# Kernel tuning notes

Hardware: AMD Instinct MI355X
Metric: run time of the kernel (lower is better)

The kernel has to match this reference:

```python
import jax, jax.numpy as jnp
import numpy as np

P = 32          # patch_size (window side); N = P*P tokens
C = 192         # dim
HEADS = 12
HD = C // HEADS # 16
HIDDEN = C * 4  # mlp_ratio=4
SCALE = HD ** -0.5


def _conv(x, w, b, pad):
    y = jax.lax.conv_general_dilated(
        x, w, window_strides=(1, 1), padding=[(pad, pad), (pad, pad)],
        dimension_numbers=("NCHW", "OIHW", "NCHW"))
    return y + b[None, :, None, None]


def setup_inputs() -> dict:
    key = jax.random.key(0)
    ks = jax.random.split(key, 8)
    B = 16
    x = jax.random.normal(ks[0], (B, P * P, C), dtype=jnp.float32)
    w1 = jax.random.normal(ks[1], (HIDDEN, C, 3, 3), dtype=jnp.float32) * 0.05
    b1 = jnp.zeros((HIDDEN,), dtype=jnp.float32)
    w2 = jax.random.normal(ks[2], (HIDDEN, HIDDEN, 1, 1), dtype=jnp.float32) * 0.05
    b2 = jnp.zeros((HIDDEN,), dtype=jnp.float32)
    w3 = jax.random.normal(ks[3], (3 * C, HIDDEN, 1, 1), dtype=jnp.float32) * 0.05
    b3 = jnp.zeros((3 * C,), dtype=jnp.float32)
    w_out = jax.random.normal(ks[4], (C, C), dtype=jnp.float32) * (C ** -0.5)
    return {"x": x, "w1": w1, "b1": b1, "w2": w2, "b2": b2,
            "w3": w3, "b3": b3, "w_out": w_out}


def reference(x, w1, b1, w2, b2, w3, b3, w_out):
    B, N, _ = x.shape
    # [B,N,C] -> [B,C,P,P] (NCHW image per window)
    xi = jnp.transpose(x.reshape(B, P, P, C), (0, 3, 1, 2))
    # F.unfold(x, P, stride=P): single block -> [B, 1, C*P*P] (C-major flatten)
    y = xi.reshape(B, 1, C * P * P)
    # LAConv.attention1: conv3x3 -> relu -> conv1x1 -> relu -> conv1x1 -> sigmoid
    a = jax.nn.relu(_conv(xi, w1, b1, 1))
    a = jax.nn.relu(_conv(a, w2, b2, 0))
    a = jax.nn.sigmoid(_conv(a, w3, b3, 0))          # [B, 3C, P, P]
    # reshape(B,3C,1,P,1,P).permute(0,2,4,3,5,1).view(B,1,P*P*3C)
    a = jnp.transpose(a.reshape(B, 3 * C, 1, P, 1, P), (0, 2, 4, 3, 5, 1))
    a = a.reshape(B, 1, P * P * 3 * C)
    qc, kc, vc = jnp.split(a, 3, axis=-1)            # each [B, 1, P*P*C]

    def to_heads(c):
        # (chunk * unfold) -> [B,P,P,C] -> [B,C,P,P] -> heads view [B,H,N,hd]
        t = jnp.transpose((c * y).reshape(B, P, P, C), (0, 3, 1, 2))
        return jnp.transpose(t.reshape(B, N, HEADS, HD), (0, 2, 1, 3))

    q = to_heads(qc) * SCALE
    k = to_heads(kc)
    v = to_heads(vc)
    attn = jax.nn.softmax(jnp.einsum("bhnd,bhmd->bhnm", q, k), axis=-1)
    o = jnp.einsum("bhnm,bhmd->bhnd", attn, v)
    o = jnp.transpose(o, (0, 2, 1, 3)).reshape(B, N, C)
    return o @ w_out.T


if __name__ == "__main__":
    out = reference(**setup_inputs())
    print(out.shape)
```

## Files before the change

kernel.cpp:

```cpp
#include <hip/hip_runtime.h>
#include <hip/hip_bf16.h>
#include <math.h>

#define B_   16
#define P_   32
#define N_   1024
#define C_   192
#define H_   12
#define HD_  16
#define HID_ 768
#define C3_  576
#define SCALE_ 0.25f

using u16 = unsigned short;
typedef __bf16 bf16x8 __attribute__((ext_vector_type(8)));
typedef float f32x4 __attribute__((ext_vector_type(4)));
typedef u16 u16x8 __attribute__((ext_vector_type(8)));
typedef u16 u16x4 __attribute__((ext_vector_type(4)));

#define MFMA16(a, b, c) __builtin_amdgcn_mfma_f32_16x16x32_bf16((a), (b), (c), 0, 0, 0)

__device__ __forceinline__ int swz(int r) { return (r + (r >> 2)) & 3; }

__device__ __forceinline__ void splitf(float v, u16& h, u16& l) {
  union { __hip_bfloat16 b; u16 u; } c1, c2;
  c1.b = __float2bfloat16(v);
  float hv = __bfloat162float(c1.b);
  c2.b = __float2bfloat16(v - hv);
  h = c1.u; l = c2.u;
}

__device__ __forceinline__ u16 bfbits(float v) {
  union { __hip_bfloat16 b; u16 u; } c; c.b = __float2bfloat16(v); return c.u;
}

__device__ __forceinline__ bf16x8 ldfrag(const u16* base, int row, int g) {
  return __builtin_bit_cast(bf16x8,
      *(const u16x8*)(base + row * 32 + ((g ^ swz(row)) << 3)));
}

__global__ __launch_bounds__(256) void pack_x_kernel(const float* __restrict__ x,
                                                     u16* __restrict__ xph,
                                                     u16* __restrict__ xpl) {
  int tid = blockIdx.x * 256 + threadIdx.x;
  int b = tid / 27744;
  int r = tid - b * 27744;
  int pp = r / 24;
  int cg = (r - pp * 24) * 8;
  int pr = pp / 34, pc = pp - pr * 34;
  float v[8] = {0.f, 0.f, 0.f, 0.f, 0.f, 0.f, 0.f, 0.f};
  if (pr >= 1 && pr <= 32 && pc >= 1 && pc <= 32) {
    const float* src = x + ((size_t)b * N_ + (pr - 1) * 32 + (pc - 1)) * C_ + cg;
    float4 v0 = *(const float4*)src;
    float4 v1 = *(const float4*)(src + 4);
    v[0] = v0.x; v[1] = v0.y; v[2] = v0.z; v[3] = v0.w;
    v[4] = v1.x; v[5] = v1.y; v[6] = v1.z; v[7] = v1.w;
  }
  u16x8 vh, vl;
#pragma unroll
  for (int i = 0; i < 8; ++i) { u16 h, l; splitf(v[i], h, l); vh[i] = h; vl[i] = l; }
  size_t o = ((size_t)b * 1156 + pp) * C_ + cg;
  *(u16x8*)&xph[o] = vh;
  *(u16x8*)&xpl[o] = vl;
}

__global__ __launch_bounds__(256) void pack_w1_kernel(const float* __restrict__ w1,
                                                      u16* __restrict__ w1h,
                                                      u16* __restrict__ w1l) {
  int tid = blockIdx.x * 256 + threadIdx.x;
  int oc = tid / C_, ic = tid - oc * C_;
  const float* src = w1 + ((size_t)oc * C_ + ic) * 9;
#pragma unroll
  for (int t9 = 0; t9 < 9; ++t9) {
    u16 h, l; splitf(src[t9], h, l);
    size_t o = (size_t)t9 * (HID_ * C_) + oc * C_ + ic;
    w1h[o] = h; w1l[o] = l;
  }
}

__global__ __launch_bounds__(256) void pack_gen_kernel(const float* __restrict__ src,
                                                       u16* __restrict__ dh,
                                                       u16* __restrict__ dl, int n8) {
  int tid = blockIdx.x * 256 + threadIdx.x;
  if (tid >= n8) return;
  const float* s = src + (size_t)tid * 8;
  float4 v0 = *(const float4*)s;
  float4 v1 = *(const float4*)(s + 4);
  float v[8] = {v0.x, v0.y, v0.z, v0.w, v1.x, v1.y, v1.z, v1.w};
  u16x8 vh, vl;
#pragma unroll
  for (int i = 0; i < 8; ++i) { u16 h, l; splitf(v[i], h, l); vh[i] = h; vl[i] = l; }
  *(u16x8*)&dh[(size_t)tid * 8] = vh;
  *(u16x8*)&dl[(size_t)tid * 8] = vl;
}

__global__ __launch_bounds__(256) void conv_mfma_kernel(
    const u16* __restrict__ xph, const u16* __restrict__ xpl,
    const u16* __restrict__ w1h, const u16* __restrict__ w1l,
    const float* __restrict__ b1, u16* __restrict__ a1h, u16* __restrict__ a1l) {
  __shared__ u16 sA[2][128 * 32];
  __shared__ u16 sB[2][128 * 32];
  int t = threadIdx.x;
  int n0 = blockIdx.x * 128, oc0 = blockIdx.y * 128, b = blockIdx.z;
  int wid = t >> 6, lane = t & 63;
  int wm = wid >> 1, wn = wid & 1;
  int g = lane >> 4, lr = lane & 15;
  f32x4 acc[4][4] = {};

  for (int tap = 0; tap < 9; ++tap) {
    int dy = tap / 3, dx = tap - dy * 3;
    const u16* wth = w1h + (size_t)tap * (HID_ * C_);
    const u16* wtl = w1l + (size_t)tap * (HID_ * C_);
    for (int ks = 0; ks < 6; ++ks) {
      int kk = ks * 32;
      __syncthreads();
#pragma unroll
      for (int i = 0; i < 2; ++i) {
        int c = t + i * 256;
        int r = c >> 2, p = c & 3;
        size_t gidx = (size_t)(oc0 + r) * C_ + kk + p * 8;
        int lidx = r * 32 + ((p ^ swz(r)) << 3);
        *(u16x8*)&sA[0][lidx] = *(const u16x8*)&wth[gidx];
        *(u16x8*)&sA[1][lidx] = *(const u16x8*)&wtl[gidx];
      }
#pragma unroll
      for (int i = 0; i < 2; ++i) {
        int c = t + i * 256;
        int r = c >> 2, p = c & 3;
        int pix = n0 + r;
        int py = pix >> 5, px = pix & 31;
        int pad = (py + dy) * 34 + (px + dx);
        size_t gidx = ((size_t)b * 1156 + pad) * C_ + kk + p * 8;
        int lidx = r * 32 + ((p ^ swz(r)) << 3);
        *(u16x8*)&sB[0][lidx] = *(const u16x8*)&xph[gidx];
        *(u16x8*)&sB[1][lidx] = *(const u16x8*)&xpl[gidx];
      }
      __syncthreads();
      bf16x8 ah[4], al[4], bh[4], bl[4];
#pragma unroll
      for (int mf = 0; mf < 4; ++mf) {
        int row = wm * 64 + mf * 16 + lr;
        ah[mf] = ldfrag(&sA[0][0], row, g);
        al[mf] = ldfrag(&sA[1][0], row, g);
      }
#pragma unroll
      for (int nf = 0; nf < 4; ++nf) {
        int row = wn * 64 + nf * 16 + lr;
        bh[nf] = ldfrag(&sB[0][0], row, g);
        bl[nf] = ldfrag(&sB[1][0], row, g);
      }
#pragma unroll
      for (int mf = 0; mf < 4; ++mf)
#pragma unroll
        for (int nf = 0; nf < 4; ++nf) {
          acc[mf][nf] = MFMA16(ah[mf], bh[nf], acc[mf][nf]);
          acc[mf][nf] = MFMA16(al[mf], bh[nf], acc[mf][nf]);
          acc[mf][nf] = MFMA16(ah[mf], bl[nf], acc[mf][nf]);
        }
    }
  }
#pragma unroll
  for (int mf = 0; mf < 4; ++mf)
#pragma unroll
    for (int nf = 0; nf < 4; ++nf) {
      int pix = n0 + wn * 64 + nf * 16 + lr;
      int oc = oc0 + wm * 64 + mf * 16 + g * 4;
      size_t oidx = ((size_t)b * N_ + pix) * HID_ + oc;
      u16x4 vh, vl;
#pragma unroll
      for (int r = 0; r < 4; ++r) {
        float v = acc[mf][nf][r] + b1[oc + r];
        v = v > 0.f ? v : 0.f;
        u16 h, l; splitf(v, h, l);
        vh[r] = h; vl[r] = l;
      }
      *(u16x4*)&a1h[oidx] = vh;
      *(u16x4*)&a1l[oidx] = vl;
    }
}

template <int ACT, int MT>
__global__ __launch_bounds__(256) void gemm_mfma_kernel(
    const u16* __restrict__ Wh, const u16* __restrict__ Wl,
    const float* __restrict__ bias,
    const u16* __restrict__ inh, const u16* __restrict__ inl,
    void* __restrict__ out0, void* __restrict__ out1, int OC, int IC) {
  constexpr int MF = MT / 32;
  __shared__ u16 sA[2][MT * 32];
  __shared__ u16 sB[2][128 * 32];
  int t = threadIdx.x;
  int n0 = blockIdx.x * 128, oc0 = blockIdx.y * MT, b = blockIdx.z;
  int wid = t >> 6, lane = t & 63;
  int wm = wid >> 1, wn = wid & 1;
  int g = lane >> 4, lr = lane & 15;
  const u16* inbh = inh + (size_t)b * N_ * IC;
  const u16* inbl = inl + (size_t)b * N_ * IC;
  f32x4 acc[MF][4] = {};

  for (int ks = 0; ks < IC / 32; ++ks) {
    int kk = ks * 32;
    __syncthreads();
    for (int c = t; c < MT * 4; c += 256) {
      int r = c >> 2, p = c & 3;
      size_t gidx = (size_t)(oc0 + r) * IC + kk + p * 8;
      int lidx = r * 32 + ((p ^ swz(r)) << 3);
      *(u16x8*)&sA[0][lidx] = *(const u16x8*)&Wh[gidx];
      *(u16x8*)&sA[1][lidx] = *(const u16x8*)&Wl[gidx];
    }
#pragma unroll
    for (int i = 0; i < 2; ++i) {
      int c = t + i * 256;
      int r = c >> 2, p = c & 3;
      size_t gidx = (size_t)(n0 + r) * IC + kk + p * 8;
      int lidx = r * 32 + ((p ^ swz(r)) << 3);
      *(u16x8*)&sB[0][lidx] = *(const u16x8*)&inbh[gidx];
      *(u16x8*)&sB[1][lidx] = *(const u16x8*)&inbl[gidx];
    }
    __syncthreads();
    bf16x8 ah[MF], al[MF], bh[4], bl[4];
#pragma unroll
    for (int mf = 0; mf < MF; ++mf) {
      int row = wm * (MT / 2) + mf * 16 + lr;
      ah[mf] = ldfrag(&sA[0][0], row, g);
      al[mf] = ldfrag(&sA[1][0], row, g);
    }
#pragma unroll
    for (int nf = 0; nf < 4; ++nf) {
      int row = wn * 64 + nf * 16 + lr;
      bh[nf] = ldfrag(&sB[0][0], row, g);
      bl[nf] = ldfrag(&sB[1][0], row, g);
    }
#pragma unroll
    for (int mf = 0; mf < MF; ++mf)
#pragma unroll
      for (int nf = 0; nf < 4; ++nf) {
        acc[mf][nf] = MFMA16(ah[mf], bh[nf], acc[mf][nf]);
        acc[mf][nf] = MFMA16(al[mf], bh[nf], acc[mf][nf]);
        acc[mf][nf] = MFMA16(ah[mf], bl[nf], acc[mf][nf]);
      }
  }
#pragma unroll
  for (int mf = 0; mf < MF; ++mf)
#pragma unroll
    for (int nf = 0; nf < 4; ++nf) {
      int pix = n0 + wn * 64 + nf * 16 + lr;
      int oc = oc0 + wm * (MT / 2) + mf * 16 + g * 4;
      size_t oidx = ((size_t)b * N_ + pix) * OC + oc;
      if constexpr (ACT == 0) {
        u16x4 vh, vl;
#pragma unroll
        for (int r = 0; r < 4; ++r) {
          float v = acc[mf][nf][r] + bias[oc + r];
          v = v > 0.f ? v : 0.f;
          u16 h, l; splitf(v, h, l);
          vh[r] = h; vl[r] = l;
        }
        *(u16x4*)&((u16*)out0)[oidx] = vh;
        *(u16x4*)&((u16*)out1)[oidx] = vl;
      } else if constexpr (ACT == 1) {
        float4 res;
        float r0 = acc[mf][nf][0] + bias[oc + 0];
        float r1 = acc[mf][nf][1] + bias[oc + 1];
        float r2 = acc[mf][nf][2] + bias[oc + 2];
        float r3 = acc[mf][nf][3] + bias[oc + 3];
        res.x = 1.f / (1.f + __expf(-r0)); res.y = 1.f / (1.f + __expf(-r1));
        res.z = 1.f / (1.f + __expf(-r2)); res.w = 1.f / (1.f + __expf(-r3));
        *(float4*)&((float*)out0)[oidx] = res;
      } else {
        float4 res;
        res.x = acc[mf][nf][0]; res.y = acc[mf][nf][1];
        res.z = acc[mf][nf][2]; res.w = acc[mf][nf][3];
        *(float4*)&((float*)out0)[oidx] = res;
      }
    }
}

__global__ __launch_bounds__(256) void qkv_gather_kernel(const float* __restrict__ a3,
                                                         const float* __restrict__ x,
                                                         u16* __restrict__ qh,
                                                         u16* __restrict__ ql,
                                                         u16* __restrict__ kh,
                                                         u16* __restrict__ kl,
                                                         u16* __restrict__ vb) {
  int idx = blockIdx.x * 256 + threadIdx.x;
  int b = idx / 196608;
  int gg = idx - b * 196608;
  int m = gg & 1023, cc = gg >> 10;
  int j = m * 192 + cc;
  float y = x[((size_t)b * N_ + (j & 1023)) * C_ + (j >> 10)];
  int n2 = gg / 192;
  int hd = gg - n2 * 192;
  size_t out_idx = (((size_t)b * H_ + (hd >> 4)) * N_ + n2) * HD_ + (hd & 15);
  const float* a3b = a3 + (size_t)b * (C3_ * N_);
  int jk = j + 196608, jv = j + 393216;
  int nq = j / 576,  chq = j - nq * 576;
  int nk = jk / 576, chk = jk - nk * 576;
  int nv = jv / 576, chv = jv - nv * 576;
  float aq = a3b[(size_t)nq * C3_ + chq];
  float ak = a3b[(size_t)nk * C3_ + chk];
  float av = a3b[(size_t)nv * C3_ + chv];
  u16 hh, ll;
  splitf(aq * y * SCALE_, hh, ll); qh[out_idx] = hh; ql[out_idx] = ll;
  splitf(ak * y, hh, ll);          kh[out_idx] = hh; kl[out_idx] = ll;
  vb[out_idx] = bfbits(av * y);
}

__global__ __launch_bounds__(256) void attn_mfma_kernel(
    const u16* __restrict__ QH, const u16* __restrict__ QL,
    const u16* __restrict__ KH, const u16* __restrict__ KL,
    const u16* __restrict__ VB, u16* __restrict__ oh, u16* __restrict__ ol) {
  __shared__ u16 sKH[128 * 32];
  __shared__ u16 sKL[128 * 32];
  __shared__ u16 sVT[16 * 128];
  __shared__ u16 sP[4][16 * 128];
  int t = threadIdx.x;
  int qt = blockIdx.x, h = blockIdx.y, b = blockIdx.z;
  int wid = t >> 6, lane = t & 63;
  int lr = lane & 15, g = lane >> 4;
  size_t base = ((size_t)(b * H_ + h)) * (N_ * HD_);
  int qrow = qt * 64 + wid * 16 + lr;

  {
    int plane = t >> 7, r = t & 127;
    u16* dst = (plane ? sKL : sKH) + r * 32;
    u16x8 z = {};
    *(u16x8*)(dst + ((2 ^ swz(r)) << 3)) = z;
    *(u16x8*)(dst + ((3 ^ swz(r)) << 3)) = z;
  }

  bf16x8 qfh = {}, qfl = {};
  if (g < 2) {
    size_t qi = base + (size_t)qrow * HD_ + g * 8;
    qfh = __builtin_bit_cast(bf16x8, *(const u16x8*)&QH[qi]);
    qfl = __builtin_bit_cast(bf16x8, *(const u16x8*)&QL[qi]);
  }

  f32x4 acc = {};
  float mrun = -1e30f, lrun = 0.f;
  u16* pw = &sP[wid][0];

  for (int ch = 0; ch < 8; ++ch) {
    int key0 = ch * 128;
    __syncthreads();
    {
      int plane = t >> 7, id = t & 127;
      const u16* kbase = (plane ? KL : KH) + base;
      u16* dstb = plane ? sKL : sKH;
#pragma unroll
      for (int i = 0; i < 2; ++i) {
        int e = i * 128 + id;
        int r = e >> 1, gg2 = e & 1;
        *(u16x8*)&dstb[r * 32 + ((gg2 ^ swz(r)) << 3)] =
            *(const u16x8*)&kbase[(size_t)(key0 + r) * HD_ + gg2 * 8];
      }
    }
#pragma unroll
    for (int i = 0; i < 2; ++i) {
      int e = i * 256 + t;
      int key = e >> 2, d0 = (e & 3) * 4;
      u16x4 vv = *(const u16x4*)&VB[base + (size_t)(key0 + key) * HD_ + d0];
#pragma unroll
      for (int jj = 0; jj < 4; ++jj) {
        int d = d0 + jj;
        sVT[d * 128 + (((key >> 3) ^ (d & 7)) << 3) + (key & 7)] = vv[jj];
      }
    }
    __syncthreads();

    f32x4 st[8];
#pragma unroll
    for (int t8 = 0; t8 < 8; ++t8) {
      bf16x8 kfh = ldfrag(sKH, t8 * 16 + lr, g);
      bf16x8 kfl = ldfrag(sKL, t8 * 16 + lr, g);
      f32x4 s = {};
      s = MFMA16(kfh, qfl, s);
      s = MFMA16(kfl, qfh, s);
      s = MFMA16(kfh, qfh, s);
      st[t8] = s;
    }

    float cmax = -1e30f;
#pragma unroll
    for (int t8 = 0; t8 < 8; ++t8)
#pragma unroll
      for (int r = 0; r < 4; ++r) cmax = fmaxf(cmax, st[t8][r]);
    cmax = fmaxf(cmax, __shfl_xor(cmax, 16));
    cmax = fmaxf(cmax, __shfl_xor(cmax, 32));
    float mnew = fmaxf(mrun, cmax);
    float corr = __expf(mrun - mnew);
    float p[32];
    float psum = 0.f;
#pragma unroll
    for (int t8 = 0; t8 < 8; ++t8)
#pragma unroll
      for (int r = 0; r < 4; ++r) {
        float pv = __expf(st[t8][r] - mnew);
        p[t8 * 4 + r] = pv; psum += pv;
      }
    psum += __shfl_xor(psum, 16);
    psum += __shfl_xor(psum, 32);
    lrun = lrun * corr + psum;
    mrun = mnew;
#pragma unroll
    for (int r = 0; r < 4; ++r) acc[r] *= corr;

#pragma unroll
    for (int t8 = 0; t8 < 8; ++t8) {
      unsigned w0 = (unsigned)bfbits(p[t8 * 4 + 0]) | ((unsigned)bfbits(p[t8 * 4 + 1]) << 16);
      unsigned w1 = (unsigned)bfbits(p[t8 * 4 + 2]) | ((unsigned)bfbits(p[t8 * 4 + 3]) << 16);
      int c = 2 * t8 + (g >> 1);
      int off = lr * 128 + ((c ^ (lr & 7)) << 3) + (g & 1) * 4;
      uint2 val; val.x = w0; val.y = w1;
      *(uint2*)&pw[off] = val;
    }
#pragma unroll
    for (int kk = 0; kk < 4; ++kk) {
      int off = lr * 128 + (((kk * 4 + g) ^ (lr & 7)) << 3);
      bf16x8 pb = __builtin_bit_cast(bf16x8, *(const u16x8*)&pw[off]);
      bf16x8 va = __builtin_bit_cast(bf16x8, *(const u16x8*)&sVT[off]);
      acc = MFMA16(va, pb, acc);
    }
  }

  float inv = 1.0f / lrun;
  size_t o = ((size_t)b * N_ + qrow) * C_ + h * HD_ + 4 * g;
  u16x4 vh, vl;
#pragma unroll
  for (int r = 0; r < 4; ++r) {
    u16 hh, ll; splitf(acc[r] * inv, hh, ll);
    vh[r] = hh; vl[r] = ll;
  }
  *(u16x4*)&oh[o] = vh;
  *(u16x4*)&ol[o] = vl;
}

extern "C" void kernel_launch(void* const* d_in, const int* in_sizes, int n_in,
                              void* d_out, int out_size, void* d_ws, size_t ws_size,
                              hipStream_t stream) {
  const float* x     = (const float*)d_in[0];
  const float* w1    = (const float*)d_in[1];
  const float* b1    = (const float*)d_in[2];
  const float* w2    = (const float*)d_in[3];
  const float* b2    = (const float*)d_in[4];
  const float* w3    = (const float*)d_in[5];
  const float* b3    = (const float*)d_in[6];
  const float* w_out = (const float*)d_in[7];
  float* out = (float*)d_out;

  char* ws = (char*)d_ws;
  u16* XPH = (u16*)(ws + 0);
  u16* XPL = (u16*)(ws + 7102464);
  u16* W1H = (u16*)(ws + 14204928);
  u16* W1L = (u16*)(ws + 16859136);
  u16* W2H = (u16*)(ws + 19513344);
  u16* W2L = (u16*)(ws + 20692992);
  u16* W3H = (u16*)(ws + 21872640);
  u16* W3L = (u16*)(ws + 22757376);
  u16* WOH = (u16*)(ws + 23642112);
  u16* WOL = (u16*)(ws + 23715840);
  u16*   A1H = (u16*)(ws + 23789568);
  u16*   A1L = (u16*)(ws + 48955392);
  float* A3  = (float*)(ws + 23789568);
  u16*   OH  = (u16*)(ws + 23789568);
  u16*   OL  = (u16*)(ws + 36372480);
  u16*   A2H = (u16*)(ws + 74121216);
  u16*   A2L = (u16*)(ws + 99287040);
  u16*   QHb = (u16*)(ws + 74121216);
  u16*   QLb = (u16*)(ws + 80412672);
  u16*   KHb = (u16*)(ws + 86704128);
  u16*   KLb = (u16*)(ws + 92995584);
  u16*   VBb = (u16*)(ws + 99287040);

  pack_x_kernel<<<dim3(1734), 256, 0, stream>>>(x, XPH, XPL);
  pack_w1_kernel<<<dim3(576), 256, 0, stream>>>(w1, W1H, W1L);
  pack_gen_kernel<<<dim3(288), 256, 0, stream>>>(w2, W2H, W2L, 73728);
  pack_gen_kernel<<<dim3(216), 256, 0, stream>>>(w3, W3H, W3L, 55296);
  pack_gen_kernel<<<dim3(18), 256, 0, stream>>>(w_out, WOH, WOL, 4608);

  conv_mfma_kernel<<<dim3(8, 6, 16), 256, 0, stream>>>(XPH, XPL, W1H, W1L, b1, A1H, A1L);
  gemm_mfma_kernel<0, 128><<<dim3(8, 6, 16), 256, 0, stream>>>(
      W2H, W2L, b2, A1H, A1L, A2H, A2L, HID_, HID_);
  gemm_mfma_kernel<1, 64><<<dim3(8, 9, 16), 256, 0, stream>>>(
      W3H, W3L, b3, A2H, A2L, A3, nullptr, C3_, HID_);
  qkv_gather_kernel<<<dim3(12288), 256, 0, stream>>>(A3, x, QHb, QLb, KHb, KLb, VBb);
  attn_mfma_kernel<<<dim3(16, 12, 16), 256, 0, stream>>>(QHb, QLb, KHb, KLb, VBb, OH, OL);
  gemm_mfma_kernel<2, 64><<<dim3(8, 3, 16), 256, 0, stream>>>(
      WOH, WOL, nullptr, OH, OL, out, nullptr, C_, C_);
}
```

Before: 498.1 us.

## Stage conv halo tile once per K-slice and read weights directly from global

The 3x3 conv kernel now loads a 6-row padded halo of the input (204 pixels) into shared memory once per 32-channel K-slice and reuses it across all 9 taps, instead of reloading a shifted input tile for every tap. Weight fragments in both the conv and the 1x1 GEMM kernels are now read straight from global memory into registers, which removes the shared-memory staging of the A operand. The conv kernel also gets a launch-bounds occupancy hint of 3 blocks per CU. The aim is fewer barriers and less global-to-LDS traffic, at the cost of uncoalesced, cache-dependent global weight loads inside the MFMA loop.

```diff
diff --git a/kernel.cpp b/kernel.cpp
--- a/kernel.cpp
+++ b/kernel.cpp
@@ -37,6 +37,10 @@
 __device__ __forceinline__ bf16x8 ldfrag(const u16* base, int row, int g) {
   return __builtin_bit_cast(bf16x8,
       *(const u16x8*)(base + row * 32 + ((g ^ swz(row)) << 3)));
+}
+
+__device__ __forceinline__ bf16x8 ldg8(const u16* p) {
+  return __builtin_bit_cast(bf16x8, *(const u16x8*)p);
 }
 
 __global__ __launch_bounds__(256) void pack_x_kernel(const float* __restrict__ x,
@@ -94,60 +98,49 @@
   *(u16x8*)&dl[(size_t)tid * 8] = vl;
 }
 
-__global__ __launch_bounds__(256) void conv_mfma_kernel(
+__global__ __launch_bounds__(256, 3) void conv_mfma_kernel(
     const u16* __restrict__ xph, const u16* __restrict__ xpl,
     const u16* __restrict__ w1h, const u16* __restrict__ w1l,
     const float* __restrict__ b1, u16* __restrict__ a1h, u16* __restrict__ a1l) {
-  __shared__ u16 sA[2][128 * 32];
-  __shared__ u16 sB[2][128 * 32];
+  __shared__ u16 sH[2][204 * 32];
   int t = threadIdx.x;
   int n0 = blockIdx.x * 128, oc0 = blockIdx.y * 128, b = blockIdx.z;
+  int row0 = blockIdx.x * 4;
   int wid = t >> 6, lane = t & 63;
   int wm = wid >> 1, wn = wid & 1;
   int g = lane >> 4, lr = lane & 15;
   f32x4 acc[4][4] = {};
 
-  for (int tap = 0; tap < 9; ++tap) {
-    int dy = tap / 3, dx = tap - dy * 3;
-    const u16* wth = w1h + (size_t)tap * (HID_ * C_);
-    const u16* wtl = w1l + (size_t)tap * (HID_ * C_);
-    for (int ks = 0; ks < 6; ++ks) {
-      int kk = ks * 32;
-      __syncthreads();
-#pragma unroll
-      for (int i = 0; i < 2; ++i) {
-        int c = t + i * 256;
-        int r = c >> 2, p = c & 3;
-        size_t gidx = (size_t)(oc0 + r) * C_ + kk + p * 8;
-        int lidx = r * 32 + ((p ^ swz(r)) << 3);
-        *(u16x8*)&sA[0][lidx] = *(const u16x8*)&wth[gidx];
-        *(u16x8*)&sA[1][lidx] = *(const u16x8*)&wtl[gidx];
-      }
-#pragma unroll
-      for (int i = 0; i < 2; ++i) {
-        int c = t + i * 256;
-        int r = c >> 2, p = c & 3;
-        int pix = n0 + r;
-        int py = pix >> 5, px = pix & 31;
-        int pad = (py + dy) * 34 + (px + dx);
-        size_t gidx = ((size_t)b * 1156 + pad) * C_ + kk + p * 8;
-        int lidx = r * 32 + ((p ^ swz(r)) << 3);
-        *(u16x8*)&sB[0][lidx] = *(const u16x8*)&xph[gidx];
-        *(u16x8*)&sB[1][lidx] = *(const u16x8*)&xpl[gidx];
-      }
-      __syncthreads();
+  for (int ks = 0; ks < 6; ++ks) {
+    int kk = ks * 32;
+    __syncthreads();
+    for (int c = t; c < 1632; c += 256) {
+      int plane = c >= 816;
+      int rem = c - plane * 816;
+      int px = rem >> 2, p = rem & 3;
+      size_t gidx = ((size_t)b * 1156 + row0 * 34 + px) * C_ + kk + p * 8;
+      const u16* src = plane ? xpl : xph;
+      *(u16x8*)&sH[plane][px * 32 + ((p ^ swz(px)) << 3)] = *(const u16x8*)&src[gidx];
+    }
+    __syncthreads();
+
+    for (int tap = 0; tap < 9; ++tap) {
+      int dy = tap / 3, dx = tap - dy * 3;
+      const u16* wth = w1h + (size_t)tap * (HID_ * C_) + kk + g * 8;
+      const u16* wtl = w1l + (size_t)tap * (HID_ * C_) + kk + g * 8;
       bf16x8 ah[4], al[4], bh[4], bl[4];
 #pragma unroll
       for (int mf = 0; mf < 4; ++mf) {
-        int row = wm * 64 + mf * 16 + lr;
-        ah[mf] = ldfrag(&sA[0][0], row, g);
-        al[mf] = ldfrag(&sA[1][0], row, g);
+        size_t arow = (size_t)(oc0 + wm * 64 + mf * 16 + lr) * C_;
+        ah[mf] = ldg8(wth + arow);
+        al[mf] = ldg8(wtl + arow);
       }
 #pragma unroll
       for (int nf = 0; nf < 4; ++nf) {
-        int row = wn * 64 + nf * 16 + lr;
-        bh[nf] = ldfrag(&sB[0][0], row, g);
-        bl[nf] = ldfrag(&sB[1][0], row, g);
+        int lp = wn * 64 + nf * 16 + lr;
+        int hpx = ((lp >> 5) + dy) * 34 + (lp & 31) + dx;
+        bh[nf] = ldfrag(&sH[0][0], hpx, g);
+        bl[nf] = ldfrag(&sH[1][0], hpx, g);
       }
 #pragma unroll
       for (int mf = 0; mf < 4; ++mf)
@@ -186,7 +179,6 @@
     const u16* __restrict__ inh, const u16* __restrict__ inl,
     void* __restrict__ out0, void* __restrict__ out1, int OC, int IC) {
   constexpr int MF = MT / 32;
-  __shared__ u16 sA[2][MT * 32];
   __shared__ u16 sB[2][128 * 32];
   int t = threadIdx.x;
   int n0 = blockIdx.x * 128, oc0 = blockIdx.y * MT, b = blockIdx.z;
@@ -200,13 +192,6 @@
   for (int ks = 0; ks < IC / 32; ++ks) {
     int kk = ks * 32;
     __syncthreads();
-    for (int c = t; c < MT * 4; c += 256) {
-      int r = c >> 2, p = c & 3;
-      size_t gidx = (size_t)(oc0 + r) * IC + kk + p * 8;
-      int lidx = r * 32 + ((p ^ swz(r)) << 3);
-      *(u16x8*)&sA[0][lidx] = *(const u16x8*)&Wh[gidx];
-      *(u16x8*)&sA[1][lidx] = *(const u16x8*)&Wl[gidx];
-    }
 #pragma unroll
     for (int i = 0; i < 2; ++i) {
       int c = t + i * 256;
@@ -220,9 +205,9 @@
     bf16x8 ah[MF], al[MF], bh[4], bl[4];
 #pragma unroll
     for (int mf = 0; mf < MF; ++mf) {
-      int row = wm * (MT / 2) + mf * 16 + lr;
-      ah[mf] = ldfrag(&sA[0][0], row, g);
-      al[mf] = ldfrag(&sA[1][0], row, g);
+      size_t ai = (size_t)(oc0 + wm * (MT / 2) + mf * 16 + lr) * IC + kk + g * 8;
+      ah[mf] = ldg8(&Wh[ai]);
+      al[mf] = ldg8(&Wl[ai]);
     }
 #pragma unroll
     for (int nf = 0; nf < 4; ++nf) {
```

Result: slower. 607.1 us (+21.9%).
